# Optimization experiments

Measured on AMD Instinct MI355X. Metric: run time of the kernel, lower is better.

Reference implementation:

```python
import jax, jax.numpy as jnp
import numpy as np

B, S, H = 8, 1024, 768
NUM_HEADS, DH = 12, 64
A, T = 12, 64

def setup_inputs() -> dict:
    key = jax.random.key(0)
    ks = jax.random.split(key, 12)
    all_tokens = jax.random.normal(ks[0], (B, S, H), dtype=jnp.float32)
    aspect_tokens = jax.random.normal(ks[1], (B, A, H), dtype=jnp.float32)
    # ragged target slices: start in [0, S-17), length in [1, 16]
    starts = jax.random.randint(ks[2], (T,), 0, S - 17)
    lens = jax.random.randint(ks[3], (T,), 1, 17)
    target_pos_info = jnp.stack([starts, starts + lens], axis=-1).astype(jnp.int32)  # (T,2)
    target_batch_info = jnp.sort(jax.random.randint(ks[4], (T,), 0, B)).astype(jnp.int32)
    attention_mask = jnp.ones((B, S), dtype=jnp.int32)
    s = 0.02
    W1 = jax.random.normal(ks[5], (H, H), dtype=jnp.float32) * s
    b1 = jnp.zeros((H,), dtype=jnp.float32)
    Wq = jax.random.normal(ks[6], (H, NUM_HEADS, DH), dtype=jnp.float32) * s
    bq = jnp.zeros((NUM_HEADS, DH), dtype=jnp.float32)
    Wk = jax.random.normal(ks[7], (H, NUM_HEADS, DH), dtype=jnp.float32) * s
    bk = jnp.zeros((NUM_HEADS, DH), dtype=jnp.float32)
    Wc = jax.random.normal(ks[8], (2 * H, 1), dtype=jnp.float32) * s
    bc = jnp.zeros((1,), dtype=jnp.float32)
    return {"all_tokens": all_tokens, "aspect_tokens": aspect_tokens,
            "target_pos_info": target_pos_info, "target_batch_info": target_batch_info,
            "attention_mask": attention_mask,
            "W1": W1, "b1": b1, "Wq": Wq, "bq": bq, "Wk": Wk, "bk": bk,
            "Wc": Wc, "bc": bc}


def reference(all_tokens, aspect_tokens, target_pos_info, target_batch_info,
              attention_mask, W1, b1, Wq, bq, Wk, bk, Wc, bc):
    # linear_transform (shared for tokens and aspects), dropout = identity at eval
    h = jax.nn.relu(jnp.einsum('bsh,hg->bsg', all_tokens, W1) + b1)     # (B,S,H)
    # SelfAttention: q/k EinsumDense projections; value = raw key_states reshaped
    q = jnp.einsum('bsh,hkd->bskd', h, Wq) + bq                          # (B,S,K,D)
    k = jnp.einsum('bsh,hkd->bskd', h, Wk) + bk
    v = h.reshape(k.shape)                                               # faithful: reshape, no proj
    q = q * jax.lax.rsqrt(jnp.asarray(DH, q.dtype))
    scores = jnp.einsum('bskd,bqkd->bkqs', k, q)                         # (B,K,Q,S)
    mask_val = attention_mask[:, 0].astype(scores.dtype)                 # original uses mask[:, 0:1]
    scores = scores + ((1.0 - mask_val) * -10000.0)[:, None, None, None]
    probs = jax.nn.softmax(scores, axis=-1)
    out = jnp.einsum('bkqs,bskd->bqkd', probs, v).reshape(h.shape)       # (B,S,H)
    # ragged per-target slice mean: masked mean over positions [s0, s1)
    pos = jnp.arange(S)
    s0, s1 = target_pos_info[:, 0], target_pos_info[:, 1]
    span = ((pos[None, :] >= s0[:, None]) & (pos[None, :] < s1[:, None])).astype(out.dtype)  # (T,S)
    gathered = out[target_batch_info]                                    # (T,S,H)
    counts = jnp.maximum(span.sum(-1, keepdims=True), 1.0)
    rep = jnp.einsum('ts,tsh->th', span, gathered) / counts              # (T,H)
    # aspect hidden states and target-aspect pairing (batch-ordered concat)
    h_a = jax.nn.relu(jnp.einsum('bah,hg->bag', aspect_tokens, W1) + b1)  # (B,A,H)
    pair = jnp.concatenate([jnp.broadcast_to(rep[:, None, :], (rep.shape[0], A, H)),
                            h_a[target_batch_info]], axis=-1)             # (T,A,2H)
    t_a_logit = jnp.einsum('tac,co->tao', pair, Wc) + bc                  # (T,A,1)
    return t_a_logit
```

## Files before the change

### kernel.cpp

```cpp
#include <hip/hip_runtime.h>


typedef __attribute__((ext_vector_type(8))) short s8v;
typedef __attribute__((ext_vector_type(4))) short s4v;
typedef __attribute__((ext_vector_type(4))) float f4v;

#define AS1 __attribute__((address_space(1)))
#define AS3 __attribute__((address_space(3)))

__device__ __forceinline__ unsigned short f2bf(float f) {
  union { float f; unsigned u; } v; v.f = f;
  unsigned r = v.u + 0x7FFFu + ((v.u >> 16) & 1u);
  return (unsigned short)(r >> 16);
}

__device__ __forceinline__ float bf2f(unsigned short u) {
  union { unsigned u; float f; } v; v.u = ((unsigned)u) << 16;
  return v.f;
}

__device__ __forceinline__ void gl2lds16(const void* g, void* l) {
  __builtin_amdgcn_global_load_lds((const AS1 void*)g, (AS3 void*)l, 16, 0, 0);
}

__global__ __launch_bounds__(256) void k_prep(const float* __restrict__ asp,
                                              const float* __restrict__ W1,
                                              const float* __restrict__ Wq,
                                              const float* __restrict__ Wk,
                                              unsigned short* __restrict__ Abf,
                                              unsigned short* __restrict__ W1t,
                                              unsigned short* __restrict__ Wqt,
                                              unsigned short* __restrict__ Wkt,
                                              float* __restrict__ outz) {
  __shared__ float T[64][68];
  int bid = blockIdx.x;
  int tid = threadIdx.x;
  if (bid < 36) {
    int i = bid * 256 + tid;
    const float4* src = (const float4*)(asp + (size_t)i * 8);
    float4 a = src[0], b = src[1];
    s8v o;
    o[0] = (short)f2bf(a.x); o[1] = (short)f2bf(a.y);
    o[2] = (short)f2bf(a.z); o[3] = (short)f2bf(a.w);
    o[4] = (short)f2bf(b.x); o[5] = (short)f2bf(b.y);
    o[6] = (short)f2bf(b.z); o[7] = (short)f2bf(b.w);
    *(s8v*)(Abf + (size_t)i * 8) = o;
  } else if (bid < 468) {
    int wb = bid - 36;
    const float* W = (wb < 144) ? W1 : (wb < 288) ? Wq : Wk;
    unsigned short* Wt = (wb < 144) ? W1t : (wb < 288) ? Wqt : Wkt;
    int tile = wb % 144;
    int tr = (tile / 12) * 64;
    int tc = (tile % 12) * 64;
#pragma unroll
    for (int p = 0; p < 4; ++p) {
      int r = p * 16 + (tid >> 4);
      int c = (tid & 15) * 4;
      float4 v = *(const float4*)(W + (size_t)(tr + r) * 768 + tc + c);
      T[r][c] = v.x; T[r][c + 1] = v.y; T[r][c + 2] = v.z; T[r][c + 3] = v.w;
    }
    __syncthreads();
#pragma unroll
    for (int p = 0; p < 2; ++p) {
      int n = p * 32 + (tid >> 3);
      int k8 = (tid & 7) * 8;
      s8v o;
#pragma unroll
      for (int j = 0; j < 8; ++j) o[j] = (short)f2bf(T[k8 + j][n]);
      *(s8v*)(Wt + (size_t)(tc + n) * 768 + tr + k8) = o;
    }
  } else {
#pragma unroll
    for (int q = 0; q < 3; ++q) outz[tid + q * 256] = 0.f;
  }
}

template <int MODE, bool AF32>
__device__ __forceinline__ void gemm_tile(int m0, int n0,
    const unsigned short* __restrict__ A, const float* __restrict__ Af,
    const unsigned short* __restrict__ Bt,
    const float* __restrict__ bias, unsigned short* __restrict__ C,
    unsigned short* __restrict__ C2, const int* __restrict__ pos,
    const int* __restrict__ tbi, unsigned short* LDSB, int* srcRow) {
  const int K = 768;
  int tid = threadIdx.x, lane = tid & 63, w = tid >> 6;

  if (MODE == 2) {
    if (tid < 128) {
      int r = m0 + tid;
      int t = r >> 4, j = r & 15;
      int s0 = pos[2 * t], s1 = pos[2 * t + 1];
      int s = s0 + j; if (s > s1 - 1) s = s1 - 1;
      srcRow[tid] = tbi[t] * 1024 + s;
    }
    __syncthreads();
  }

  int rsub = lane >> 3;
  int cXor = ((lane & 7) ^ rsub) * 8;
  const unsigned short* aSrc[4];
  const float* aSrcF[4];
  const unsigned short* bSrc[4];
#pragma unroll
  for (int i = 0; i < 4; ++i) {
    int lr = (w * 4 + i) * 8 + rsub;
    size_t grow;
    if (MODE == 2) grow = (size_t)srcRow[lr];
    else if (MODE == 3) { int rr = m0 + lr; grow = (size_t)(rr < 96 ? rr : 95); }
    else grow = (size_t)(m0 + lr);
    if (AF32) aSrcF[i] = Af + grow * K + cXor;
    else aSrc[i] = A + grow * K + cXor;
    bSrc[i] = Bt + (size_t)(n0 + lr) * K + cXor;
  }

  f4v acc[4][4];
#pragma unroll
  for (int i = 0; i < 4; ++i)
#pragma unroll
    for (int j = 0; j < 4; ++j) acc[i][j] = (f4v)(0.0f);

  int wm = (w >> 1) * 64, wn = (w & 1) * 64;
  int lc = lane & 15, lg = lane >> 4;
  int aIdx[4][2], bIdx[4][2];
#pragma unroll
  for (int mi = 0; mi < 4; ++mi) {
    int ra = wm + mi * 16 + lc;
    int rb = wn + mi * 16 + lc;
#pragma unroll
    for (int kk = 0; kk < 2; ++kk) {
      aIdx[mi][kk] = ra * 64 + (((kk * 4 + lg) ^ (ra & 7)) * 8);
      bIdx[mi][kk] = rb * 64 + (((kk * 4 + lg) ^ (rb & 7)) * 8);
    }
  }

  if (AF32) {
    float4 p0[4], p1[4];
#pragma unroll
    for (int i = 0; i < 4; ++i) {
      const float* p = aSrcF[i];
      p0[i] = *(const float4*)p;
      p1[i] = *(const float4*)(p + 4);
    }
#pragma unroll
    for (int i = 0; i < 4; ++i) gl2lds16(bSrc[i], LDSB + 8192 + (w * 4 + i) * 512);
#pragma unroll
    for (int i = 0; i < 4; ++i) {
      s8v o;
      o[0] = (short)f2bf(p0[i].x); o[1] = (short)f2bf(p0[i].y);
      o[2] = (short)f2bf(p0[i].z); o[3] = (short)f2bf(p0[i].w);
      o[4] = (short)f2bf(p1[i].x); o[5] = (short)f2bf(p1[i].y);
      o[6] = (short)f2bf(p1[i].z); o[7] = (short)f2bf(p1[i].w);
      *(s8v*)(LDSB + (w * 4 + i) * 512 + lane * 8) = o;
    }
  } else {
#pragma unroll
    for (int i = 0; i < 4; ++i) gl2lds16(aSrc[i], LDSB + (w * 4 + i) * 512);
#pragma unroll
    for (int i = 0; i < 4; ++i) gl2lds16(bSrc[i], LDSB + 8192 + (w * 4 + i) * 512);
  }
  asm volatile("s_waitcnt vmcnt(0)" ::: "memory");
  __builtin_amdgcn_s_barrier();

  for (int t = 0; t < 12; ++t) {
    int cur = t & 1;
    unsigned short* Acur = LDSB + cur * 16384;
    unsigned short* Bcur = Acur + 8192;
    unsigned short* Anxt = LDSB + (cur ^ 1) * 16384;
    unsigned short* Bnxt = Anxt + 8192;
    bool pf = (t < 11);
    int k1 = (t + 1) * 64;
    float4 av0[4], av1[4];
    if (pf) {
      if (AF32) {
#pragma unroll
        for (int i = 0; i < 4; ++i) {
          const float* p = aSrcF[i] + k1;
          av0[i] = *(const float4*)p;
          av1[i] = *(const float4*)(p + 4);
        }
      } else {
#pragma unroll
        for (int i = 0; i < 4; ++i) gl2lds16(aSrc[i] + k1, Anxt + (w * 4 + i) * 512);
      }
#pragma unroll
      for (int i = 0; i < 4; ++i) gl2lds16(bSrc[i] + k1, Bnxt + (w * 4 + i) * 512);
    }
#pragma unroll
    for (int kk = 0; kk < 2; ++kk) {
      s8v ar[4], br[4];
#pragma unroll
      for (int mi = 0; mi < 4; ++mi) ar[mi] = *(const s8v*)(Acur + aIdx[mi][kk]);
#pragma unroll
      for (int ni = 0; ni < 4; ++ni) br[ni] = *(const s8v*)(Bcur + bIdx[ni][kk]);
#pragma unroll
      for (int mi = 0; mi < 4; ++mi)
#pragma unroll
        for (int ni = 0; ni < 4; ++ni)
          acc[mi][ni] = __builtin_amdgcn_mfma_f32_16x16x32_bf16(ar[mi], br[ni], acc[mi][ni], 0, 0, 0);
    }
    if (pf) {
      if (AF32) {
#pragma unroll
        for (int i = 0; i < 4; ++i) {
          s8v o;
          o[0] = (short)f2bf(av0[i].x); o[1] = (short)f2bf(av0[i].y);
          o[2] = (short)f2bf(av0[i].z); o[3] = (short)f2bf(av0[i].w);
          o[4] = (short)f2bf(av1[i].x); o[5] = (short)f2bf(av1[i].y);
          o[6] = (short)f2bf(av1[i].z); o[7] = (short)f2bf(av1[i].w);
          *(s8v*)(Anxt + (w * 4 + i) * 512 + lane * 8) = o;
        }
      }
      asm volatile("s_waitcnt vmcnt(0)" ::: "memory");
      __builtin_amdgcn_s_barrier();
    }
  }

  if (MODE == 0 || MODE == 1) {
    unsigned short* L = LDSB;
#pragma unroll
    for (int mi = 0; mi < 4; ++mi) {
#pragma unroll
      for (int ni = 0; ni < 4; ++ni) {
        int coll = wn + ni * 16 + lc;
        float bv = bias[n0 + coll];
        int row0l = wm + mi * 16 + lg * 4;
        s4v pk;
#pragma unroll
        for (int r = 0; r < 4; ++r) {
          float x = acc[mi][ni][r] + bv;
          if (MODE == 0) x = x > 0.f ? x : 0.f;
          unsigned short hv = f2bf(x);
          pk[r] = (short)hv;
          int rowl = row0l + r;
          L[rowl * 128 + (((coll >> 3) ^ (rowl & 7)) * 8) + (coll & 7)] = hv;
        }
        if (MODE == 0) {
          int grow0 = m0 + row0l;
          int b = grow0 >> 10, s = grow0 & 1023;
          int gcol = n0 + coll;
          int kh = gcol >> 6, d = gcol & 63;
          *(s4v*)(C2 + ((size_t)((b * 12 + kh) * 64 + d)) * 1024 + s) = pk;
        }
      }
    }
    __syncthreads();
#pragma unroll
    for (int p = 0; p < 8; ++p) {
      int rowl = p * 16 + (tid >> 4);
      int cs = (tid & 15) * 8;
      int chunk = (cs >> 3) ^ (rowl & 7);
      s8v v = *(const s8v*)(L + rowl * 128 + chunk * 8);
      if (MODE == 0) {
        *(s8v*)(C + (size_t)(m0 + rowl) * 768 + n0 + cs) = v;
      } else {
        int gr = m0 + rowl;
        int b = gr >> 10, s = gr & 1023;
        int gcol = n0 + cs;
        int kh = gcol >> 6, d = gcol & 63;
        *(s8v*)(C + ((size_t)((b * 12 + kh) * 1024 + s)) * 64 + d) = v;
      }
    }
  } else {
#pragma unroll
    for (int mi = 0; mi < 4; ++mi) {
#pragma unroll
      for (int ni = 0; ni < 4; ++ni) {
        int col = n0 + wn + ni * 16 + lc;
        float bv = bias[col];
        int row0 = m0 + wm + mi * 16 + lg * 4;
#pragma unroll
        for (int r = 0; r < 4; ++r) {
          int row = row0 + r;
          float x = acc[mi][ni][r] + bv;
          if (MODE == 2) {
            x *= 0.125f;
            int t = row >> 4, j = row & 15;
            int kh = col >> 6, d = col & 63;
            C[(size_t)((t * 12 + kh) * 16 + j) * 64 + d] = f2bf(x);
          } else {
            x = x > 0.f ? x : 0.f;
            if (row < 96) C[(size_t)row * 768 + col] = f2bf(x);
          }
        }
      }
    }
  }
}

__global__ __launch_bounds__(256) void k_gemmA(const float* __restrict__ X,
                                               const float* __restrict__ asp,
                                               const unsigned short* __restrict__ W1t,
                                               const float* __restrict__ b1,
                                               unsigned short* __restrict__ Hbf,
                                               unsigned short* __restrict__ Vt,
                                               unsigned short* __restrict__ Ha) {
  __shared__ unsigned short LDSB[32768];
  __shared__ int srcRow[128];
  int bid = blockIdx.x;
  if (bid < 384) {
    bid = (bid & 7) * 48 + (bid >> 3);
    gemm_tile<0, true>((bid / 6) * 128, (bid % 6) * 128, (const unsigned short*)nullptr,
                       X, W1t, b1, Hbf, Vt, (const int*)nullptr, (const int*)nullptr,
                       LDSB, srcRow);
  } else {
    int b2 = bid - 384;
    gemm_tile<3, true>(0, b2 * 128, (const unsigned short*)nullptr,
                       asp, W1t, b1, Ha, (unsigned short*)nullptr,
                       (const int*)nullptr, (const int*)nullptr, LDSB, srcRow);
  }
}

__global__ __launch_bounds__(256) void k_gemmB(const unsigned short* __restrict__ Hbf,
                                               const unsigned short* __restrict__ Wkt,
                                               const float* __restrict__ bk,
                                               unsigned short* __restrict__ Khm,
                                               const unsigned short* __restrict__ Wqt,
                                               const float* __restrict__ bq,
                                               unsigned short* __restrict__ Qhm,
                                               const int* __restrict__ pos,
                                               const int* __restrict__ tbi) {
  __shared__ unsigned short LDSB[32768];
  __shared__ int srcRow[128];
  int bid = blockIdx.x;
  bid = (bid & 7) * 54 + (bid >> 3);
  if (bid < 384) {
    gemm_tile<1, false>((bid / 6) * 128, (bid % 6) * 128, Hbf, (const float*)nullptr,
                        Wkt, bk, Khm, (unsigned short*)nullptr,
                        (const int*)nullptr, (const int*)nullptr, LDSB, srcRow);
  } else {
    int b2 = bid - 384;
    gemm_tile<2, false>((b2 / 6) * 128, (b2 % 6) * 128, Hbf, (const float*)nullptr,
                        Wqt, bq, Qhm, (unsigned short*)nullptr, pos, tbi,
                        LDSB, srcRow);
  }
}

__global__ __launch_bounds__(256) void k_attn(const unsigned short* __restrict__ q_hm,
                                              const unsigned short* __restrict__ k_hm,
                                              const unsigned short* __restrict__ vt,
                                              const unsigned short* __restrict__ ha,
                                              const int* __restrict__ pos,
                                              const int* __restrict__ tbi,
                                              const float* __restrict__ Wc,
                                              const float* __restrict__ bc,
                                              float* __restrict__ outp) {
  __shared__ unsigned short P[16 * 1032];
  __shared__ float O[4][16][64];
  __shared__ float rsbuf[4][16];
  __shared__ float inv_rs[16];
  __shared__ float hpart[4];
  __shared__ float rabuf;

  int bid = blockIdx.x;
  bid = (bid & 7) * 96 + (bid >> 3);
  int t = bid / 12, kh = bid % 12;
  int b = tbi[t];
  int s0 = pos[2 * t], s1 = pos[2 * t + 1];
  int len = s1 - s0;
  int tid = threadIdx.x, lane = tid & 63, w = tid >> 6;
  int lg = lane >> 4, lc = lane & 15;

  const unsigned short* qb = q_hm + (size_t)((t * 12 + kh) * 16) * 64;
  s8v a0 = *(const s8v*)(qb + (size_t)lc * 64 + lg * 8);
  s8v a1 = *(const s8v*)(qb + (size_t)lc * 64 + 32 + lg * 8);

  const unsigned short* kb = k_hm + (size_t)((b * 12 + kh) * 1024) * 64;
  float rs[4] = {0.f, 0.f, 0.f, 0.f};
  for (int it = 0; it < 16; ++it) {
    int sb = it * 64 + w * 16;
    s8v b0 = *(const s8v*)(kb + (size_t)(sb + lc) * 64 + lg * 8);
    s8v b1 = *(const s8v*)(kb + (size_t)(sb + lc) * 64 + 32 + lg * 8);
    f4v c = (f4v)(0.0f);
    c = __builtin_amdgcn_mfma_f32_16x16x32_bf16(a0, b0, c, 0, 0, 0);
    c = __builtin_amdgcn_mfma_f32_16x16x32_bf16(a1, b1, c, 0, 0, 0);
#pragma unroll
    for (int r = 0; r < 4; ++r) {
      float p = __expf(c[r]);
      rs[r] += p;
      P[(lg * 4 + r) * 1032 + sb + lc] = f2bf(p);
    }
  }
#pragma unroll
  for (int m = 1; m < 16; m <<= 1) {
#pragma unroll
    for (int r = 0; r < 4; ++r) rs[r] += __shfl_xor(rs[r], m, 64);
  }
  if (lc == 0) {
#pragma unroll
    for (int r = 0; r < 4; ++r) rsbuf[w][lg * 4 + r] = rs[r];
  }
  __syncthreads();
  if (tid < 16)
    inv_rs[tid] = 1.0f / (rsbuf[0][tid] + rsbuf[1][tid] + rsbuf[2][tid] + rsbuf[3][tid]);

  const unsigned short* vb = vt + (size_t)((b * 12 + kh) * 64) * 1024;
  f4v oc[4];
#pragma unroll
  for (int n = 0; n < 4; ++n) oc[n] = (f4v)(0.0f);
  for (int it = 0; it < 8; ++it) {
    int s32 = it * 128 + w * 32;
    s8v pa = *(const s8v*)(P + lc * 1032 + s32 + lg * 8);
#pragma unroll
    for (int n = 0; n < 4; ++n) {
      s8v vbf = *(const s8v*)(vb + (size_t)(n * 16 + lc) * 1024 + s32 + lg * 8);
      oc[n] = __builtin_amdgcn_mfma_f32_16x16x32_bf16(pa, vbf, oc[n], 0, 0, 0);
    }
  }
#pragma unroll
  for (int n = 0; n < 4; ++n)
#pragma unroll
    for (int r = 0; r < 4; ++r) O[w][lg * 4 + r][n * 16 + lc] = oc[n][r];
  __syncthreads();
  if (w == 0) {
    float sum = 0.f;
    for (int j = 0; j < len; ++j) {
      float v = O[0][j][lane] + O[1][j][lane] + O[2][j][lane] + O[3][j][lane];
      sum += v * inv_rs[j];
    }
    float repd = sum / (float)len;
    float pr = repd * Wc[kh * 64 + lane];
#pragma unroll
    for (int m = 1; m < 64; m <<= 1) pr += __shfl_xor(pr, m, 64);
    if (lane == 0) rabuf = pr;
  } else {
    const unsigned short* hr = ha + (size_t)(b * 12 + kh) * 768;
    float p2 = 0.f;
#pragma unroll
    for (int q = 0; q < 4; ++q) {
      int g = (tid - 64) + q * 192;
      p2 += bf2f(hr[g]) * Wc[768 + g];
    }
#pragma unroll
    for (int m = 1; m < 64; m <<= 1) p2 += __shfl_xor(p2, m, 64);
    if (lane == 0) hpart[w] = p2;
  }
  __syncthreads();
  if (tid < 12) {
    float ra = rabuf;
    float had = hpart[1] + hpart[2] + hpart[3];
    float v = ra + ((tid == kh) ? (had + bc[0]) : 0.f);
    atomicAdd(&outp[t * 12 + tid], v);
  }
}

extern "C" void kernel_launch(void* const* d_in, const int* in_sizes, int n_in,
                              void* d_out, int out_size, void* d_ws, size_t ws_size,
                              hipStream_t stream) {
  const float* all_tokens = (const float*)d_in[0];
  const float* aspect     = (const float*)d_in[1];
  const int*   pos        = (const int*)d_in[2];
  const int*   tbi        = (const int*)d_in[3];
  const float* W1 = (const float*)d_in[5];
  const float* b1 = (const float*)d_in[6];
  const float* Wq = (const float*)d_in[7];
  const float* bq = (const float*)d_in[8];
  const float* Wk = (const float*)d_in[9];
  const float* bk = (const float*)d_in[10];
  const float* Wc = (const float*)d_in[11];
  const float* bc = (const float*)d_in[12];
  float* out = (float*)d_out;

  char* ws = (char*)d_ws;
  unsigned short* W1t = (unsigned short*)(ws + 12582912);
  unsigned short* Wqt = (unsigned short*)(ws + 13762560);
  unsigned short* Wkt = (unsigned short*)(ws + 14942208);
  unsigned short* Hbf = (unsigned short*)(ws + 16121856);
  unsigned short* Khm = (unsigned short*)(ws + 28704768);
  unsigned short* Vt  = (unsigned short*)(ws + 41287680);
  unsigned short* Qhm = (unsigned short*)(ws + 53870592);
  unsigned short* Abf = (unsigned short*)(ws + 55640448);
  unsigned short* Ha  = (unsigned short*)(ws + 55787904);

  hipLaunchKernelGGL(k_prep, dim3(469), dim3(256), 0, stream,
                     aspect, W1, Wq, Wk, Abf, W1t, Wqt, Wkt, out);
  hipLaunchKernelGGL(k_gemmA, dim3(390), dim3(256), 0, stream,
                     all_tokens, aspect, W1t, b1, Hbf, Vt, Ha);
  hipLaunchKernelGGL(k_gemmB, dim3(432), dim3(256), 0, stream,
                     Hbf, Wkt, bk, Khm, Wqt, bq, Qhm, pos, tbi);
  hipLaunchKernelGGL(k_attn, dim3(768), dim3(256), 0, stream,
                     Qhm, Khm, Vt, Ha, pos, tbi, Wc, bc, out);
}
```

Measured before the change: 79.64 us.

## Pre-convert token matrix to bf16 in prep kernel and use async LDS loads

The fp32 all_tokens matrix is now converted to bf16 in the prep kernel, writing it to workspace, instead of being converted inside the first GEMM's A-tile loads. This lets the GEMM use direct global-to-LDS loads for A as well as B, removing register staging and the conversion work from the main loop. The K-loop synchronisation is also restructured to wait for only part of the outstanding loads and to use two barriers per iteration. The trade-off is an extra full pass over the 25MB token array (fp32 read plus bf16 write and re-read) in a separate kernel.

```diff
diff --git a/kernel.cpp b/kernel.cpp
--- a/kernel.cpp
+++ b/kernel.cpp
@@ -23,10 +23,12 @@
   __builtin_amdgcn_global_load_lds((const AS1 void*)g, (AS3 void*)l, 16, 0, 0);
 }
 
-__global__ __launch_bounds__(256) void k_prep(const float* __restrict__ asp,
+__global__ __launch_bounds__(256) void k_prep(const float* __restrict__ X,
+                                              const float* __restrict__ asp,
                                               const float* __restrict__ W1,
                                               const float* __restrict__ Wq,
                                               const float* __restrict__ Wk,
+                                              unsigned short* __restrict__ Xbf,
                                               unsigned short* __restrict__ Abf,
                                               unsigned short* __restrict__ W1t,
                                               unsigned short* __restrict__ Wqt,
@@ -35,8 +37,18 @@
   __shared__ float T[64][68];
   int bid = blockIdx.x;
   int tid = threadIdx.x;
-  if (bid < 36) {
+  if (bid < 3072) {
     int i = bid * 256 + tid;
+    const float4* src = (const float4*)(X + (size_t)i * 8);
+    float4 a = src[0], b = src[1];
+    s8v o;
+    o[0] = (short)f2bf(a.x); o[1] = (short)f2bf(a.y);
+    o[2] = (short)f2bf(a.z); o[3] = (short)f2bf(a.w);
+    o[4] = (short)f2bf(b.x); o[5] = (short)f2bf(b.y);
+    o[6] = (short)f2bf(b.z); o[7] = (short)f2bf(b.w);
+    *(s8v*)(Xbf + (size_t)i * 8) = o;
+  } else if (bid < 3108) {
+    int i = (bid - 3072) * 256 + tid;
     const float4* src = (const float4*)(asp + (size_t)i * 8);
     float4 a = src[0], b = src[1];
     s8v o;
@@ -45,8 +57,8 @@
     o[4] = (short)f2bf(b.x); o[5] = (short)f2bf(b.y);
     o[6] = (short)f2bf(b.z); o[7] = (short)f2bf(b.w);
     *(s8v*)(Abf + (size_t)i * 8) = o;
-  } else if (bid < 468) {
-    int wb = bid - 36;
+  } else if (bid < 3540) {
+    int wb = bid - 3108;
     const float* W = (wb < 144) ? W1 : (wb < 288) ? Wq : Wk;
     unsigned short* Wt = (wb < 144) ? W1t : (wb < 288) ? Wqt : Wkt;
     int tile = wb % 144;
@@ -75,10 +87,9 @@
   }
 }
 
-template <int MODE, bool AF32>
+template <int MODE>
 __device__ __forceinline__ void gemm_tile(int m0, int n0,
-    const unsigned short* __restrict__ A, const float* __restrict__ Af,
-    const unsigned short* __restrict__ Bt,
+    const unsigned short* __restrict__ A, const unsigned short* __restrict__ Bt,
     const float* __restrict__ bias, unsigned short* __restrict__ C,
     unsigned short* __restrict__ C2, const int* __restrict__ pos,
     const int* __restrict__ tbi, unsigned short* LDSB, int* srcRow) {
@@ -99,7 +110,6 @@
   int rsub = lane >> 3;
   int cXor = ((lane & 7) ^ rsub) * 8;
   const unsigned short* aSrc[4];
-  const float* aSrcF[4];
   const unsigned short* bSrc[4];
 #pragma unroll
   for (int i = 0; i < 4; ++i) {
@@ -108,8 +118,7 @@
     if (MODE == 2) grow = (size_t)srcRow[lr];
     else if (MODE == 3) { int rr = m0 + lr; grow = (size_t)(rr < 96 ? rr : 95); }
     else grow = (size_t)(m0 + lr);
-    if (AF32) aSrcF[i] = Af + grow * K + cXor;
-    else aSrc[i] = A + grow * K + cXor;
+    aSrc[i] = A + grow * K + cXor;
     bSrc[i] = Bt + (size_t)(n0 + lr) * K + cXor;
   }
 
@@ -133,31 +142,10 @@
     }
   }
 
-  if (AF32) {
-    float4 p0[4], p1[4];
-#pragma unroll
-    for (int i = 0; i < 4; ++i) {
-      const float* p = aSrcF[i];
-      p0[i] = *(const float4*)p;
-      p1[i] = *(const float4*)(p + 4);
-    }
-#pragma unroll
-    for (int i = 0; i < 4; ++i) gl2lds16(bSrc[i], LDSB + 8192 + (w * 4 + i) * 512);
-#pragma unroll
-    for (int i = 0; i < 4; ++i) {
-      s8v o;
-      o[0] = (short)f2bf(p0[i].x); o[1] = (short)f2bf(p0[i].y);
-      o[2] = (short)f2bf(p0[i].z); o[3] = (short)f2bf(p0[i].w);
-      o[4] = (short)f2bf(p1[i].x); o[5] = (short)f2bf(p1[i].y);
-      o[6] = (short)f2bf(p1[i].z); o[7] = (short)f2bf(p1[i].w);
-      *(s8v*)(LDSB + (w * 4 + i) * 512 + lane * 8) = o;
-    }
-  } else {
-#pragma unroll
-    for (int i = 0; i < 4; ++i) gl2lds16(aSrc[i], LDSB + (w * 4 + i) * 512);
-#pragma unroll
-    for (int i = 0; i < 4; ++i) gl2lds16(bSrc[i], LDSB + 8192 + (w * 4 + i) * 512);
-  }
+#pragma unroll
+  for (int i = 0; i < 4; ++i) gl2lds16(aSrc[i], LDSB + (w * 4 + i) * 512);
+#pragma unroll
+  for (int i = 0; i < 4; ++i) gl2lds16(bSrc[i], LDSB + 8192 + (w * 4 + i) * 512);
   asm volatile("s_waitcnt vmcnt(0)" ::: "memory");
   __builtin_amdgcn_s_barrier();
 
@@ -165,26 +153,17 @@
     int cur = t & 1;
     unsigned short* Acur = LDSB + cur * 16384;
     unsigned short* Bcur = Acur + 8192;
-    unsigned short* Anxt = LDSB + (cur ^ 1) * 16384;
-    unsigned short* Bnxt = Anxt + 8192;
-    bool pf = (t < 11);
-    int k1 = (t + 1) * 64;
-    float4 av0[4], av1[4];
-    if (pf) {
-      if (AF32) {
-#pragma unroll
-        for (int i = 0; i < 4; ++i) {
-          const float* p = aSrcF[i] + k1;
-          av0[i] = *(const float4*)p;
-          av1[i] = *(const float4*)(p + 4);
-        }
-      } else {
-#pragma unroll
-        for (int i = 0; i < 4; ++i) gl2lds16(aSrc[i] + k1, Anxt + (w * 4 + i) * 512);
-      }
+    if (t < 11) {
+      unsigned short* Anxt = LDSB + (cur ^ 1) * 16384;
+      unsigned short* Bnxt = Anxt + 8192;
+      int k1 = (t + 1) * 64;
+#pragma unroll
+      for (int i = 0; i < 4; ++i) gl2lds16(aSrc[i] + k1, Anxt + (w * 4 + i) * 512);
 #pragma unroll
       for (int i = 0; i < 4; ++i) gl2lds16(bSrc[i] + k1, Bnxt + (w * 4 + i) * 512);
-    }
+      asm volatile("s_waitcnt vmcnt(8)" ::: "memory");
+    }
+    __builtin_amdgcn_s_barrier();
 #pragma unroll
     for (int kk = 0; kk < 2; ++kk) {
       s8v ar[4], br[4];
@@ -198,21 +177,7 @@
         for (int ni = 0; ni < 4; ++ni)
           acc[mi][ni] = __builtin_amdgcn_mfma_f32_16x16x32_bf16(ar[mi], br[ni], acc[mi][ni], 0, 0, 0);
     }
-    if (pf) {
-      if (AF32) {
-#pragma unroll
-        for (int i = 0; i < 4; ++i) {
-          s8v o;
-          o[0] = (short)f2bf(av0[i].x); o[1] = (short)f2bf(av0[i].y);
-          o[2] = (short)f2bf(av0[i].z); o[3] = (short)f2bf(av0[i].w);
-          o[4] = (short)f2bf(av1[i].x); o[5] = (short)f2bf(av1[i].y);
-          o[6] = (short)f2bf(av1[i].z); o[7] = (short)f2bf(av1[i].w);
-          *(s8v*)(Anxt + (w * 4 + i) * 512 + lane * 8) = o;
-        }
-      }
-      asm volatile("s_waitcnt vmcnt(0)" ::: "memory");
-      __builtin_amdgcn_s_barrier();
-    }
+    __builtin_amdgcn_s_barrier();
   }
 
   if (MODE == 0 || MODE == 1) {
@@ -287,8 +252,8 @@
   }
 }
 
-__global__ __launch_bounds__(256) void k_gemmA(const float* __restrict__ X,
-                                               const float* __restrict__ asp,
+__global__ __launch_bounds__(256) void k_gemmA(const unsigned short* __restrict__ Xbf,
+                                               const unsigned short* __restrict__ Abf,
                                                const unsigned short* __restrict__ W1t,
                                                const float* __restrict__ b1,
                                                unsigned short* __restrict__ Hbf,
@@ -299,14 +264,12 @@
   int bid = blockIdx.x;
   if (bid < 384) {
     bid = (bid & 7) * 48 + (bid >> 3);
-    gemm_tile<0, true>((bid / 6) * 128, (bid % 6) * 128, (const unsigned short*)nullptr,
-                       X, W1t, b1, Hbf, Vt, (const int*)nullptr, (const int*)nullptr,
-                       LDSB, srcRow);
+    gemm_tile<0>((bid / 6) * 128, (bid % 6) * 128, Xbf, W1t, b1, Hbf, Vt,
+                 (const int*)nullptr, (const int*)nullptr, LDSB, srcRow);
   } else {
     int b2 = bid - 384;
-    gemm_tile<3, true>(0, b2 * 128, (const unsigned short*)nullptr,
-                       asp, W1t, b1, Ha, (unsigned short*)nullptr,
-                       (const int*)nullptr, (const int*)nullptr, LDSB, srcRow);
+    gemm_tile<3>(0, b2 * 128, Abf, W1t, b1, Ha, (unsigned short*)nullptr,
+                 (const int*)nullptr, (const int*)nullptr, LDSB, srcRow);
   }
 }
 
@@ -324,14 +287,13 @@
   int bid = blockIdx.x;
   bid = (bid & 7) * 54 + (bid >> 3);
   if (bid < 384) {
-    gemm_tile<1, false>((bid / 6) * 128, (bid % 6) * 128, Hbf, (const float*)nullptr,
-                        Wkt, bk, Khm, (unsigned short*)nullptr,
-                        (const int*)nullptr, (const int*)nullptr, LDSB, srcRow);
+    gemm_tile<1>((bid / 6) * 128, (bid % 6) * 128, Hbf, Wkt, bk, Khm,
+                 (unsigned short*)nullptr, (const int*)nullptr, (const int*)nullptr,
+                 LDSB, srcRow);
   } else {
     int b2 = bid - 384;
-    gemm_tile<2, false>((b2 / 6) * 128, (b2 % 6) * 128, Hbf, (const float*)nullptr,
-                        Wqt, bq, Qhm, (unsigned short*)nullptr, pos, tbi,
-                        LDSB, srcRow);
+    gemm_tile<2>((b2 / 6) * 128, (b2 % 6) * 128, Hbf, Wqt, bq, Qhm,
+                 (unsigned short*)nullptr, pos, tbi, LDSB, srcRow);
   }
 }
 
@@ -461,6 +423,7 @@
   float* out = (float*)d_out;
 
   char* ws = (char*)d_ws;
+  unsigned short* Xbf = (unsigned short*)(ws);
   unsigned short* W1t = (unsigned short*)(ws + 12582912);
   unsigned short* Wqt = (unsigned short*)(ws + 13762560);
   unsigned short* Wkt = (unsigned short*)(ws + 14942208);
@@ -471,10 +434,10 @@
   unsigned short* Abf = (unsigned short*)(ws + 55640448);
   unsigned short* Ha  = (unsigned short*)(ws + 55787904);
 
-  hipLaunchKernelGGL(k_prep, dim3(469), dim3(256), 0, stream,
-                     aspect, W1, Wq, Wk, Abf, W1t, Wqt, Wkt, out);
+  hipLaunchKernelGGL(k_prep, dim3(3541), dim3(256), 0, stream,
+                     all_tokens, aspect, W1, Wq, Wk, Xbf, Abf, W1t, Wqt, Wkt, out);
   hipLaunchKernelGGL(k_gemmA, dim3(390), dim3(256), 0, stream,
-                     all_tokens, aspect, W1t, b1, Hbf, Vt, Ha);
+                     Xbf, Abf, W1t, b1, Hbf, Vt, Ha);
   hipLaunchKernelGGL(k_gemmB, dim3(432), dim3(256), 0, stream,
                      Hbf, Wkt, bk, Khm, Wqt, bq, Qhm, pos, tbi);
   hipLaunchKernelGGL(k_attn, dim3(768), dim3(256), 0, stream,
```

Result: no change. 79.40 us (-0.3%).
